# Kernel tuning notes

Hardware: AMD Instinct MI355X
Metric: run time of the kernel (lower is better)

The kernel has to match this reference:

```python
import jax, jax.numpy as jnp
import numpy as np

LN_EPS = 1e-5
NEG_INF = -1e38


def wkv_scan(w, u, k, v):
    """Numerically-stable RWKV WKV recurrence (matches wkv_cuda forward).
    w: [C] (negative decay), u: [C] bonus, k/v: [B,T,C]. Returns y: [B,T,C]."""
    Bdim, T, C = k.shape

    def step(carry, kv_t):
        p, q, o = carry  # running num, den, log-scale, each [B,C]
        kt, vt = kv_t
        no = jnp.maximum(o, u + kt)
        A = jnp.exp(o - no)
        Bw = jnp.exp(u + kt - no)
        y = (A * p + Bw * vt) / (A * q + Bw)
        no2 = jnp.maximum(w + o, kt)
        A2 = jnp.exp(w + o - no2)
        B2 = jnp.exp(kt - no2)
        return (A2 * p + B2 * vt, A2 * q + B2, no2), y

    init = (jnp.zeros((Bdim, C), k.dtype), jnp.zeros((Bdim, C), k.dtype),
            jnp.full((Bdim, C), NEG_INF, k.dtype))
    kT = jnp.moveaxis(k, 1, 0)  # [T,B,C]
    vT = jnp.moveaxis(v, 1, 0)
    _, ys = jax.lax.scan(step, init, (kT, vT))
    return jnp.moveaxis(ys, 0, 1)  # [B,T,C]


def setup_inputs() -> dict:
    key = jax.random.key(0)
    ks = jax.random.split(key, 8)
    B, C, H, W = 16, 192, 56, 56
    s = 0.02
    x = jax.random.normal(ks[0], (B, C, H, W), jnp.float32)
    Wk = jax.random.normal(ks[1], (C, C), jnp.float32) * s
    Wv = jax.random.normal(ks[2], (C, C), jnp.float32) * s
    Wr = jax.random.normal(ks[3], (C, C), jnp.float32) * s
    Wo = jax.random.normal(ks[4], (C, C), jnp.float32) * s
    ln_g = jnp.ones((C,), jnp.float32)
    ln_b = jnp.zeros((C,), jnp.float32)
    w_decay = -6.0 + 0.1 * jax.random.normal(ks[5], (C,), jnp.float32)
    u = 0.1 * jax.random.normal(ks[6], (C,), jnp.float32)
    return {"x": x, "Wk": Wk, "Wv": Wv, "Wr": Wr, "Wo": Wo,
            "ln_g": ln_g, "ln_b": ln_b, "w_decay": w_decay, "u": u}


def reference(x, Wk, Wv, Wr, Wo, ln_g, ln_b, w_decay, u):
    B, C, H, W = x.shape
    xs = jnp.transpose(x.reshape(B, C, H * W), (0, 2, 1))  # [B,T,C]
    k = jnp.einsum('btc,dc->btd', xs, Wk)
    v = jnp.einsum('btc,dc->btd', xs, Wv)
    r = jnp.einsum('btc,dc->btd', xs, Wr)
    real_w = -jnp.exp(w_decay)
    x_fwd = wkv_scan(real_w, u, k, v)
    x_bwd = jnp.flip(wkv_scan(real_w, u, jnp.flip(k, 1), jnp.flip(v, 1)), 1)
    x_bi = 0.5 * (x_fwd + x_bwd)
    h = jax.nn.sigmoid(r) * x_bi
    mu = jnp.mean(h, axis=-1, keepdims=True)
    var = jnp.var(h, axis=-1, keepdims=True)
    h = (h - mu) * jax.lax.rsqrt(var + LN_EPS) * ln_g + ln_b
    out = jnp.einsum('btc,dc->btd', h, Wo)  # dropout is identity at eval
    return jnp.transpose(out, (0, 2, 1)).reshape(B, C, H, W)
```

## Files before the change

kernel.cpp:

```cpp
#include <hip/hip_runtime.h>

#define BB 16
#define CC 192
#define TPIX 3136
#define NCH 49
#define CHL 64
#define NNELE ((size_t)BB * TPIX * CC)
#define NSTATE ((size_t)2 * BB * NCH * CC)
#define WCH (CC * CC)

typedef __attribute__((ext_vector_type(8))) short bf16x8;
typedef __attribute__((ext_vector_type(4))) short bf16x4;
typedef __attribute__((ext_vector_type(4))) float f32x4;
typedef __attribute__((ext_vector_type(16))) float f32x16;

__device__ __forceinline__ unsigned short f2bf(float f) {
    union { float f; unsigned u; } v; v.f = f;
    unsigned r = v.u + 0x7FFFu + ((v.u >> 16) & 1u);
    return (unsigned short)(r >> 16);
}
__device__ __forceinline__ float bf2f(unsigned short h) {
    union { unsigned u; float f; } v; v.u = ((unsigned)h) << 16;
    return v.f;
}


__global__ __launch_bounds__(256) void wcvt_frag(
    const float* __restrict__ Wk, const float* __restrict__ Wv,
    const float* __restrict__ Wr, const float* __restrict__ Wo,
    unsigned short* __restrict__ wfrag)
{
    const int id = blockIdx.x * 256 + threadIdx.x;
    const int m = id / 4608;
    const int r = id % 4608;
    const int tile = r >> 6;
    const int lane = r & 63;
    const int dr = tile / 12, tk = tile % 12;
    const int d = dr * 32 + (lane & 31);
    const int c = tk * 16 + (lane >> 5) * 8;
    const float* W = (m == 0) ? Wk : (m == 1) ? Wv : (m == 2) ? Wr : Wo;
    const float4 a = *(const float4*)&W[d * CC + c];
    const float4 b = *(const float4*)&W[d * CC + c + 4];
    bf16x8 o;
    o[0] = (short)f2bf(a.x); o[1] = (short)f2bf(a.y);
    o[2] = (short)f2bf(a.z); o[3] = (short)f2bf(a.w);
    o[4] = (short)f2bf(b.x); o[5] = (short)f2bf(b.y);
    o[6] = (short)f2bf(b.z); o[7] = (short)f2bf(b.w);
    *(bf16x8*)&wfrag[(size_t)m * WCH + (size_t)tile * 512 + lane * 8] = o;
}

__global__ __launch_bounds__(256) void xcvt_frag(
    const float* __restrict__ x, unsigned short* __restrict__ xfrag)
{
    const int t0 = blockIdx.x * 32;
    const int b  = blockIdx.y;
    __shared__ float ls[CC][33];
    const int tid = threadIdx.x;
#pragma unroll
    for (int it = 0; it < 6; ++it) {
        const int c  = it * 32 + (tid >> 3);
        const int t4 = (tid & 7) * 4;
        *(float4*)&ls[c][t4] =
            *(const float4*)&x[((size_t)b * CC + c) * TPIX + t0 + t4];
    }
    __syncthreads();
    const size_t tbase = ((size_t)(b * TPIX + t0) >> 5) * 12;
#pragma unroll
    for (int it = 0; it < 3; ++it) {
        const int id = it * 256 + tid;
        const int tk = id >> 6;
        const int lane = id & 63;
        const int r32 = lane & 31;
        const int c0 = tk * 16 + (lane >> 5) * 8;
        bf16x8 o;
#pragma unroll
        for (int e = 0; e < 8; ++e)
            o[e] = (short)f2bf(ls[c0 + e][r32]);
        *(bf16x8*)&xfrag[(tbase + tk) * 512 + lane * 8] = o;
    }
}

__global__ __launch_bounds__(256) void proj_mfma32(
    const unsigned short* __restrict__ xfrag,
    const unsigned short* __restrict__ wfrag,
    unsigned short* __restrict__ kbf, unsigned short* __restrict__ vbf,
    unsigned short* __restrict__ rbf)
{
    const int lane = threadIdx.x & 63;
    const int wv   = threadIdx.x >> 6;
    const int tw   = wv >> 1;
    const int dwav = wv & 1;
    const size_t row0 = (size_t)blockIdx.x * 64 + tw * 32;
    const int l31 = lane & 31;
    const int kh  = lane >> 5;
    const int m   = blockIdx.z;

    const unsigned short* wm = wfrag + (size_t)m * WCH;
    const size_t xtb = (row0 >> 5) * 12;

    f32x16 acc[3];
#pragma unroll
    for (int nn = 0; nn < 3; ++nn)
#pragma unroll
        for (int e = 0; e < 16; ++e) acc[nn][e] = 0.f;

#pragma unroll
    for (int ks = 0; ks < 12; ++ks) {
        const bf16x8 xf = *(const bf16x8*)&xfrag[(xtb + ks) * 512 + lane * 8];
        bf16x8 wf[3];
#pragma unroll
        for (int nn = 0; nn < 3; ++nn)
            wf[nn] = *(const bf16x8*)&wm[(size_t)((dwav * 3 + nn) * 12 + ks) * 512 + lane * 8];
#pragma unroll
        for (int nn = 0; nn < 3; ++nn)
            acc[nn] = __builtin_amdgcn_mfma_f32_32x32x16_bf16(
                wf[nn], xf, acc[nn], 0, 0, 0);
    }

    unsigned short* om = (m == 0) ? kbf : (m == 1) ? vbf : rbf;
    const size_t trow = (row0 + l31) * CC + dwav * 96 + 4 * kh;
#pragma unroll
    for (int nn = 0; nn < 3; ++nn)
#pragma unroll
        for (int q2 = 0; q2 < 4; ++q2) {
            bf16x4 pk;
#pragma unroll
            for (int j = 0; j < 4; ++j)
                pk[j] = (short)f2bf(acc[nn][q2 * 4 + j]);
            *(bf16x4*)&om[trow + nn * 32 + 8 * q2] = pk;
        }
}

__global__ __launch_bounds__(256) void outproj_mfma32(
    const unsigned short* __restrict__ hfrag,
    const unsigned short* __restrict__ wo,
    float* __restrict__ out)
{
    const int lane = threadIdx.x & 63;
    const int wv   = threadIdx.x >> 6;
    const int tw   = wv >> 1;
    const int dwav = wv & 1;
    const size_t row0 = (size_t)blockIdx.x * 64 + tw * 32;
    const int l31 = lane & 31;
    const int kh  = lane >> 5;

    const size_t htb = (row0 >> 5) * 12;

    f32x16 acc[3];
#pragma unroll
    for (int nn = 0; nn < 3; ++nn)
#pragma unroll
        for (int e = 0; e < 16; ++e) acc[nn][e] = 0.f;

#pragma unroll
    for (int ks = 0; ks < 12; ++ks) {
        const bf16x8 hf = *(const bf16x8*)&hfrag[(htb + ks) * 512 + lane * 8];
        bf16x8 wf[3];
#pragma unroll
        for (int nn = 0; nn < 3; ++nn)
            wf[nn] = *(const bf16x8*)&wo[(size_t)((dwav * 3 + nn) * 12 + ks) * 512 + lane * 8];
#pragma unroll
        for (int nn = 0; nn < 3; ++nn)
            acc[nn] = __builtin_amdgcn_mfma_f32_32x32x16_bf16(
                hf, wf[nn], acc[nn], 0, 0, 0);
    }

    const int b  = (int)(row0 / TPIX);
    const int t0 = (int)(row0 % TPIX);
#pragma unroll
    for (int nn = 0; nn < 3; ++nn) {
        const int d = dwav * 96 + nn * 32 + l31;
#pragma unroll
        for (int q2 = 0; q2 < 4; ++q2) {
            const int tl = t0 + 4 * kh + 8 * q2;
            f32x4 v4 = {acc[nn][q2 * 4 + 0], acc[nn][q2 * 4 + 1],
                        acc[nn][q2 * 4 + 2], acc[nn][q2 * 4 + 3]};
            *(f32x4*)&out[((size_t)b * CC + d) * TPIX + tl] = v4;
        }
    }
}

__global__ __launch_bounds__(256) void wkv_chunk_kernel(
    const unsigned short* __restrict__ kb, const unsigned short* __restrict__ vb,
    const float* __restrict__ wdec,
    float* __restrict__ sp, float* __restrict__ sq, float* __restrict__ so)
{
    const int gid = blockIdx.x * 256 + threadIdx.x;
    const int c  = gid % CC;
    const int r  = gid / CC;
    const int ch = r % NCH;
    const int r2 = r / NCH;
    const int b  = r2 % BB;
    const int dir = r2 / BB;

    const float w = -__expf(wdec[c]);
    const int tstart = dir ? (TPIX - 1 - ch * CHL) : (ch * CHL);
    const long stride = dir ? -(long)CC : (long)CC;
    long idx = ((long)b * TPIX + tstart) * CC + c;

    float p = 0.f, q = 0.f, o = -1e38f;
#pragma unroll 4
    for (int j = 0; j < CHL; ++j) {
        const float kt = bf2f(kb[idx]), vt = bf2f(vb[idx]);
        const float wo  = w + o;
        const float no2 = fmaxf(wo, kt);
        const float A2  = __expf(wo - no2);
        const float B2  = __expf(kt - no2);
        p = A2 * p + B2 * vt;
        q = A2 * q + B2;
        o = no2;
        idx += stride;
    }
    sp[gid] = p; sq[gid] = q; so[gid] = o;
}

__global__ __launch_bounds__(256) void wkv_prefix_kernel(
    float* __restrict__ sp, float* __restrict__ sq, float* __restrict__ so,
    const float* __restrict__ wdec)
{
    const int tid = blockIdx.x * 256 + threadIdx.x;
    if (tid >= 2 * BB * CC) return;
    const int c = tid % CC;
    const int g = tid / CC;
    const float w  = -__expf(wdec[c]);
    const float wL = w * CHL;

    float P = 0.f, Q = 0.f, O = -1e38f;
    size_t idx = (size_t)g * NCH * CC + c;
    for (int ch = 0; ch < NCH; ++ch) {
        const float pl = sp[idx], ql = sq[idx], ol = so[idx];
        sp[idx] = P; sq[idx] = Q; so[idx] = O;
        const float Ow = O + wL;
        const float no = fmaxf(Ow, ol);
        const float A  = __expf(Ow - no);
        const float Bf = __expf(ol - no);
        P = A * P + Bf * pl;
        Q = A * Q + Bf * ql;
        O = no;
        idx += CC;
    }
}

__global__ __launch_bounds__(256) void wkv_emit_kernel(
    const unsigned short* __restrict__ kb, const unsigned short* __restrict__ vb,
    const float* __restrict__ wdec, const float* __restrict__ ubias,
    const float* __restrict__ sp, const float* __restrict__ sq,
    const float* __restrict__ so,
    unsigned short* __restrict__ yfwd, unsigned short* __restrict__ ybwd)
{
    const int gid = blockIdx.x * 256 + threadIdx.x;
    const int c  = gid % CC;
    const int r  = gid / CC;
    const int ch = r % NCH;
    const int r2 = r / NCH;
    const int b  = r2 % BB;
    const int dir = r2 / BB;

    const float w = -__expf(wdec[c]);
    const float u = ubias[c];
    const int tstart = dir ? (TPIX - 1 - ch * CHL) : (ch * CHL);
    const long stride = dir ? -(long)CC : (long)CC;
    long idx = ((long)b * TPIX + tstart) * CC + c;
    unsigned short* yout = dir ? ybwd : yfwd;

    float p = sp[gid], q = sq[gid], o = so[gid];
#pragma unroll 2
    for (int j = 0; j < CHL; ++j) {
        const float kt = bf2f(kb[idx]), vt = bf2f(vb[idx]);
        const float uk  = u + kt;
        const float no  = fmaxf(o, uk);
        const float A   = __expf(o - no);
        const float Bw  = __expf(uk - no);
        const float num = A * p + Bw * vt;
        const float den = A * q + Bw;
        yout[idx] = f2bf(0.5f * __fdividef(num, den));
        const float wo  = w + o;
        const float no2 = fmaxf(wo, kt);
        const float A2  = __expf(wo - no2);
        const float B2  = __expf(kt - no2);
        p = A2 * p + B2 * vt;
        q = A2 * q + B2;
        o = no2;
        idx += stride;
    }
}

__global__ __launch_bounds__(192) void ln_kernel(
    const unsigned short* __restrict__ rbf,
    const unsigned short* __restrict__ yfwd, const unsigned short* __restrict__ ybwd,
    const float* __restrict__ gamma, const float* __restrict__ beta,
    unsigned short* __restrict__ hfrag)
{
    const size_t row = blockIdx.x;
    const int c = threadIdx.x;
    const size_t idx = row * CC + c;
    const float rv = bf2f(rbf[idx]);
    const float xb = bf2f(yfwd[idx]) + bf2f(ybwd[idx]);
    const float hv = xb / (1.f + __expf(-rv));
    float s = hv, s2 = hv * hv;
#pragma unroll
    for (int off = 1; off < 64; off <<= 1) {
        s  += __shfl_xor(s, off);
        s2 += __shfl_xor(s2, off);
    }
    __shared__ float red[2][3];
    const int wv = threadIdx.x >> 6;
    if ((threadIdx.x & 63) == 0) { red[0][wv] = s; red[1][wv] = s2; }
    __syncthreads();
    s  = red[0][0] + red[0][1] + red[0][2];
    s2 = red[1][0] + red[1][1] + red[1][2];
    const float mu   = s * (1.f / CC);
    const float var  = s2 * (1.f / CC) - mu * mu;
    const float rstd = rsqrtf(var + 1e-5f);
    const float hval = (hv - mu) * rstd * gamma[c] + beta[c];
    const size_t off = ((row >> 5) * 12 + (c >> 4)) * 512 +
                       ((row & 31) + ((c >> 3) & 1) * 32) * 8 + (c & 7);
    hfrag[off] = f2bf(hval);
}

extern "C" void kernel_launch(void* const* d_in, const int* in_sizes, int n_in,
                              void* d_out, int out_size, void* d_ws, size_t ws_size,
                              hipStream_t stream)
{
    const float* x    = (const float*)d_in[0];
    const float* Wk   = (const float*)d_in[1];
    const float* Wv   = (const float*)d_in[2];
    const float* Wr   = (const float*)d_in[3];
    const float* Wo   = (const float*)d_in[4];
    const float* ln_g = (const float*)d_in[5];
    const float* ln_b = (const float*)d_in[6];
    const float* wdec = (const float*)d_in[7];
    const float* u    = (const float*)d_in[8];

    unsigned short* kbf   = (unsigned short*)d_ws;
    unsigned short* vbf   = kbf + NNELE;
    unsigned short* rbf   = vbf + NNELE;
    unsigned short* xfrag = rbf + NNELE;
    unsigned short* wfrag = xfrag + NNELE;
    float* sp = (float*)xfrag;
    float* sq = sp + NSTATE;
    float* so = sq + NSTATE;
    unsigned short* hfrag = kbf;
    unsigned short* yfwd  = (unsigned short*)d_out;
    unsigned short* ybwd  = yfwd + NNELE;
    float* out = (float*)d_out;

    wcvt_frag<<<72, 256, 0, stream>>>(Wk, Wv, Wr, Wo, wfrag);
    xcvt_frag<<<dim3(TPIX / 32, BB), 256, 0, stream>>>(x, xfrag);

    proj_mfma32<<<dim3((BB * TPIX) / 64, 1, 3), 256, 0, stream>>>(
        xfrag, wfrag, kbf, vbf, rbf);

    const int nth = (int)NSTATE;
    wkv_chunk_kernel<<<nth / 256, 256, 0, stream>>>(kbf, vbf, wdec, sp, sq, so);
    wkv_prefix_kernel<<<(2 * BB * CC + 255) / 256, 256, 0, stream>>>(sp, sq, so, wdec);
    wkv_emit_kernel<<<nth / 256, 256, 0, stream>>>(kbf, vbf, wdec, u, sp, sq, so, yfwd, ybwd);

    ln_kernel<<<BB * TPIX, 192, 0, stream>>>(rbf, yfwd, ybwd, ln_g, ln_b, hfrag);

    outproj_mfma32<<<(BB * TPIX) / 64, 256, 0, stream>>>(hfrag, wfrag + 3 * WCH, out);
}
```

Measured before the change: 151.2 us.

## Stage weight fragments in LDS and double the row tile of projection GEMMs

Both projection GEMM kernels now copy the whole 192x192 bf16 weight matrix (72 KB) into shared memory once per block and read the MFMA B-fragments from LDS instead of global memory. Blocks grow to 512 threads covering 128 rows, and the activation fragment for the next k-step is loaded one iteration ahead. The output projection now recomputes batch and pixel index per row group, because a 128-row tile can cross a batch boundary. The aim is to cut repeated global and L2 weight traffic, at the cost of a per-block copy-and-sync prologue and 72 KB of LDS per block, which limits occupancy.

```diff
diff --git a/kernel.cpp b/kernel.cpp
--- a/kernel.cpp
+++ b/kernel.cpp
@@ -80,23 +80,32 @@
     }
 }
 
-__global__ __launch_bounds__(256) void proj_mfma32(
+__global__ __launch_bounds__(512) void proj_mfma32(
     const unsigned short* __restrict__ xfrag,
     const unsigned short* __restrict__ wfrag,
     unsigned short* __restrict__ kbf, unsigned short* __restrict__ vbf,
     unsigned short* __restrict__ rbf)
 {
-    const int lane = threadIdx.x & 63;
-    const int wv   = threadIdx.x >> 6;
+    __shared__ unsigned short wlds[WCH];
+    const int tid  = threadIdx.x;
+    const int lane = tid & 63;
+    const int wv   = tid >> 6;
     const int tw   = wv >> 1;
     const int dwav = wv & 1;
-    const size_t row0 = (size_t)blockIdx.x * 64 + tw * 32;
-    const int l31 = lane & 31;
-    const int kh  = lane >> 5;
-    const int m   = blockIdx.z;
+    const int l31  = lane & 31;
+    const int kh   = lane >> 5;
+    const int m    = blockIdx.z;
 
     const unsigned short* wm = wfrag + (size_t)m * WCH;
-    const size_t xtb = (row0 >> 5) * 12;
+#pragma unroll
+    for (int it = 0; it < 9; ++it) {
+        const int off = (it * 512 + tid) * 8;
+        *(bf16x8*)&wlds[off] = *(const bf16x8*)&wm[off];
+    }
+    __syncthreads();
+
+    const size_t row0 = (size_t)blockIdx.x * 128 + tw * 32;
+    const size_t xtb  = (row0 >> 5) * 12;
 
     f32x16 acc[3];
 #pragma unroll
@@ -104,17 +113,21 @@
 #pragma unroll
         for (int e = 0; e < 16; ++e) acc[nn][e] = 0.f;
 
+    bf16x8 xf = *(const bf16x8*)&xfrag[xtb * 512 + lane * 8];
 #pragma unroll
     for (int ks = 0; ks < 12; ++ks) {
-        const bf16x8 xf = *(const bf16x8*)&xfrag[(xtb + ks) * 512 + lane * 8];
+        bf16x8 nxf;
+        if (ks < 11)
+            nxf = *(const bf16x8*)&xfrag[(xtb + ks + 1) * 512 + lane * 8];
         bf16x8 wf[3];
 #pragma unroll
         for (int nn = 0; nn < 3; ++nn)
-            wf[nn] = *(const bf16x8*)&wm[(size_t)((dwav * 3 + nn) * 12 + ks) * 512 + lane * 8];
+            wf[nn] = *(const bf16x8*)&wlds[((dwav * 3 + nn) * 12 + ks) * 512 + lane * 8];
 #pragma unroll
         for (int nn = 0; nn < 3; ++nn)
             acc[nn] = __builtin_amdgcn_mfma_f32_32x32x16_bf16(
                 wf[nn], xf, acc[nn], 0, 0, 0);
+        if (ks < 11) xf = nxf;
     }
 
     unsigned short* om = (m == 0) ? kbf : (m == 1) ? vbf : rbf;
@@ -131,20 +144,29 @@
         }
 }
 
-__global__ __launch_bounds__(256) void outproj_mfma32(
+__global__ __launch_bounds__(512) void outproj_mfma32(
     const unsigned short* __restrict__ hfrag,
     const unsigned short* __restrict__ wo,
     float* __restrict__ out)
 {
-    const int lane = threadIdx.x & 63;
-    const int wv   = threadIdx.x >> 6;
+    __shared__ unsigned short wlds[WCH];
+    const int tid  = threadIdx.x;
+    const int lane = tid & 63;
+    const int wv   = tid >> 6;
     const int tw   = wv >> 1;
     const int dwav = wv & 1;
-    const size_t row0 = (size_t)blockIdx.x * 64 + tw * 32;
-    const int l31 = lane & 31;
-    const int kh  = lane >> 5;
-
-    const size_t htb = (row0 >> 5) * 12;
+    const int l31  = lane & 31;
+    const int kh   = lane >> 5;
+
+#pragma unroll
+    for (int it = 0; it < 9; ++it) {
+        const int off = (it * 512 + tid) * 8;
+        *(bf16x8*)&wlds[off] = *(const bf16x8*)&wo[off];
+    }
+    __syncthreads();
+
+    const size_t row0 = (size_t)blockIdx.x * 128 + tw * 32;
+    const size_t htb  = (row0 >> 5) * 12;
 
     f32x16 acc[3];
 #pragma unroll
@@ -152,27 +174,31 @@
 #pragma unroll
         for (int e = 0; e < 16; ++e) acc[nn][e] = 0.f;
 
+    bf16x8 hf = *(const bf16x8*)&hfrag[htb * 512 + lane * 8];
 #pragma unroll
     for (int ks = 0; ks < 12; ++ks) {
-        const bf16x8 hf = *(const bf16x8*)&hfrag[(htb + ks) * 512 + lane * 8];
+        bf16x8 nhf;
+        if (ks < 11)
+            nhf = *(const bf16x8*)&hfrag[(htb + ks + 1) * 512 + lane * 8];
         bf16x8 wf[3];
 #pragma unroll
         for (int nn = 0; nn < 3; ++nn)
-            wf[nn] = *(const bf16x8*)&wo[(size_t)((dwav * 3 + nn) * 12 + ks) * 512 + lane * 8];
+            wf[nn] = *(const bf16x8*)&wlds[((dwav * 3 + nn) * 12 + ks) * 512 + lane * 8];
 #pragma unroll
         for (int nn = 0; nn < 3; ++nn)
             acc[nn] = __builtin_amdgcn_mfma_f32_32x32x16_bf16(
                 hf, wf[nn], acc[nn], 0, 0, 0);
-    }
-
-    const int b  = (int)(row0 / TPIX);
-    const int t0 = (int)(row0 % TPIX);
+        if (ks < 11) hf = nhf;
+    }
+
 #pragma unroll
     for (int nn = 0; nn < 3; ++nn) {
         const int d = dwav * 96 + nn * 32 + l31;
 #pragma unroll
         for (int q2 = 0; q2 < 4; ++q2) {
-            const int tl = t0 + 4 * kh + 8 * q2;
+            const size_t grow = row0 + 4 * kh + 8 * q2;
+            const int b  = (int)(grow / TPIX);
+            const int tl = (int)(grow % TPIX);
             f32x4 v4 = {acc[nn][q2 * 4 + 0], acc[nn][q2 * 4 + 1],
                         acc[nn][q2 * 4 + 2], acc[nn][q2 * 4 + 3]};
             *(f32x4*)&out[((size_t)b * CC + d) * TPIX + tl] = v4;
@@ -348,7 +374,7 @@
     wcvt_frag<<<72, 256, 0, stream>>>(Wk, Wv, Wr, Wo, wfrag);
     xcvt_frag<<<dim3(TPIX / 32, BB), 256, 0, stream>>>(x, xfrag);
 
-    proj_mfma32<<<dim3((BB * TPIX) / 64, 1, 3), 256, 0, stream>>>(
+    proj_mfma32<<<dim3((BB * TPIX) / 128, 1, 3), 512, 0, stream>>>(
         xfrag, wfrag, kbf, vbf, rbf);
 
     const int nth = (int)NSTATE;
@@ -358,5 +384,5 @@
 
     ln_kernel<<<BB * TPIX, 192, 0, stream>>>(rbf, yfwd, ybwd, ln_g, ln_b, hfrag);
 
-    outproj_mfma32<<<(BB * TPIX) / 64, 256, 0, stream>>>(hfrag, wfrag + 3 * WCH, out);
-}
+    outproj_mfma32<<<(BB * TPIX) / 128, 512, 0, stream>>>(hfrag, wfrag + 3 * WCH, out);
+}
```

Result: no change. 151.6 us (+0.3%).
